# Kernel optimization log

Hardware: AMD Instinct MI355X
Metric: run time of the kernel (lower is better)

The kernel has to match this reference:

```python
import jax, jax.numpy as jnp
import numpy as np

B, T, C = 8, 1024, 768
H, D = 12, 64

def setup_inputs() -> dict:
    key = jax.random.key(0)
    ks = jax.random.split(key, 6)
    s = 0.02
    return {
        "x": jax.random.normal(ks[0], (B, T, C), dtype=jnp.float32),
        "Wq": jax.random.normal(ks[1], (H, C, D), dtype=jnp.float32) * s,
        "Wk": jax.random.normal(ks[2], (H, C, D), dtype=jnp.float32) * s,
        "Wv": jax.random.normal(ks[3], (H, C, D), dtype=jnp.float32) * s,
        "Wproj": jax.random.normal(ks[4], (C, C), dtype=jnp.float32) * s,
        "bproj": jnp.zeros((C,), dtype=jnp.float32),
    }

def reference(x, Wq, Wk, Wv, Wproj, bproj):
    # per-head projections, vectorized over heads: [B,H,T,D]
    q = jnp.einsum('btc,hcd->bhtd', x, Wq)
    k = jnp.einsum('btc,hcd->bhtd', x, Wk)
    v = jnp.einsum('btc,hcd->bhtd', x, Wv)
    scale = 1.0 / jnp.sqrt(jnp.asarray(q.shape[-1], q.dtype))
    scores = jnp.einsum('bhtd,bhsd->bhts', q, k) * scale  # [B,H,T,T]
    attn = jax.nn.softmax(scores, axis=-1)
    out = jnp.einsum('bhts,bhsd->bhtd', attn, v)          # [B,H,T,D]
    # concat heads along last dim -> [B,T,H*D]
    out = out.transpose(0, 2, 1, 3).reshape(x.shape[0], x.shape[1], -1)
    return out @ Wproj + bproj
```

## Files before the change

### kernel.cpp

```cpp
#include <hip/hip_runtime.h>
#include <hip/hip_bf16.h>

using u16 = unsigned short;

typedef __attribute__((ext_vector_type(8))) short bf16x8;
typedef __attribute__((ext_vector_type(4))) float f32x4;
typedef __attribute__((ext_vector_type(16))) float f32x16;

#define B_ 8
#define T_ 1024
#define C_ 768
#define H_ 12
#define D_ 64

typedef const void __attribute__((address_space(1))) gv_t;
typedef void __attribute__((address_space(3))) lv_t;

__device__ __forceinline__ void gload_lds16(const void* g, void* l) {
  __builtin_amdgcn_global_load_lds((gv_t*)g, (lv_t*)l, 16, 0, 0);
}

__device__ __forceinline__ u16 f2b(float f) {
  union { float f; unsigned u; } a; a.f = f;
  unsigned r = a.u + 0x7FFFu + ((a.u >> 16) & 1u);
  return (u16)(r >> 16);
}

__device__ __forceinline__ unsigned cvtpk_bf16(float lo, float hi) {
  unsigned r;
  asm("v_cvt_pk_bf16_f32 %0, %1, %2" : "=v"(r) : "v"(lo), "v"(hi));
  return r;
}
__device__ __forceinline__ void plane32_swap(unsigned &a, unsigned &b) {
  asm volatile("v_permlane32_swap_b32 %0, %1" : "+v"(a), "+v"(b));
}

__global__ __launch_bounds__(256) void prep_all(
    const float* __restrict__ x,
    const float* __restrict__ Wq, const float* __restrict__ Wk,
    const float* __restrict__ Wv, const float* __restrict__ Wp,
    u16* __restrict__ Xb, u16* __restrict__ Wqkvt, u16* __restrict__ Wpt)
{
  int bb = blockIdx.x;
  if (bb < 3072) {
    int i = (bb * 256 + threadIdx.x) * 8;
    float4 a = *(const float4*)(x + i);
    float4 b = *(const float4*)(x + i + 4);
    union { bf16x8 v; u16 s[8]; } o;
    o.s[0] = f2b(a.x); o.s[1] = f2b(a.y); o.s[2] = f2b(a.z); o.s[3] = f2b(a.w);
    o.s[4] = f2b(b.x); o.s[5] = f2b(b.y); o.s[6] = f2b(b.z); o.s[7] = f2b(b.w);
    *(bf16x8*)(Xb + i) = o.v;
  } else {
    int idx = (bb - 3072) * 256 + threadIdx.x;
    int p = idx / 589824;
    int r = idx - p * 589824;
    int n = r / 768, c = r - n * 768;
    if (p < 3) {
      const float* W = (p == 0) ? Wq : ((p == 1) ? Wk : Wv);
      int h = n >> 6, d = n & 63;
      Wqkvt[idx] = f2b(W[(size_t)h * (C_ * D_) + (size_t)c * D_ + d]);
    } else {
      Wpt[r] = f2b(Wp[(size_t)c * 768 + n]);
    }
  }
}

#define GEMM_MAINLOOP(APTR, BPTR, KDIM)                                          \
  for (int k0 = 0; k0 < (KDIM); k0 += 64) {                                      \
    _Pragma("unroll")                                                            \
    for (int q = 0; q < 4; ++q) {                                                \
      int db = q * 4096 + t * 16;                                                \
      int row = db >> 7;                                                         \
      int cb = (db ^ ((row & 7) << 4)) & 127;                                    \
      gload_lds16((const char*)(APTR) + ((size_t)(m0 + row) * (KDIM) + k0) * 2 + cb, \
                  (char*)As + db);                                               \
      gload_lds16((const char*)(BPTR) + ((size_t)(n0 + row) * (KDIM) + k0) * 2 + cb, \
                  (char*)Bs + db);                                               \
    }                                                                            \
    asm volatile("s_waitcnt vmcnt(0)" ::: "memory");                             \
    __syncthreads();                                                             \
    _Pragma("unroll")                                                            \
    for (int kq = 0; kq < 2; ++kq) {                                             \
      bf16x8 af[4], bfr[4];                                                      \
      _Pragma("unroll")                                                          \
      for (int i = 0; i < 4; ++i) {                                              \
        int ra = wr + i * 16 + lr;                                               \
        int Ua = ra * 128 + kq * 64 + hc;                                        \
        af[i] = *(const bf16x8*)((const char*)As + (Ua ^ ((ra & 7) << 4)));      \
        int rb = wc + i * 16 + lr;                                               \
        int Ub = rb * 128 + kq * 64 + hc;                                        \
        bfr[i] = *(const bf16x8*)((const char*)Bs + (Ub ^ ((rb & 7) << 4)));     \
      }                                                                          \
      _Pragma("unroll")                                                          \
      for (int i = 0; i < 4; ++i)                                                \
        _Pragma("unroll")                                                        \
        for (int j = 0; j < 4; ++j)                                              \
          acc[i][j] = __builtin_amdgcn_mfma_f32_16x16x32_bf16(af[i], bfr[j],     \
                                                              acc[i][j], 0, 0, 0); \
    }                                                                            \
    __syncthreads();                                                             \
  }

__global__ __launch_bounds__(256) void gemm_qkv(
    const u16* __restrict__ X, const u16* __restrict__ Wt,
    u16* __restrict__ Qw, u16* __restrict__ Kw, u16* __restrict__ Vt)
{
  __shared__ __align__(16) u16 As[128 * 64];
  __shared__ __align__(16) u16 Bs[128 * 64];
  const int t = threadIdx.x;
  const int l = t & 63, w = t >> 6;
  const int lr = l & 15;
  const int hc = (l >> 4) * 16;
  const int m0 = blockIdx.x * 128;
  const int n0 = blockIdx.y * 128;
  const int wr = (w >> 1) * 64, wc = (w & 1) * 64;

  f32x4 acc[4][4] = {};
  GEMM_MAINLOOP(X, Wt, 768)

  #pragma unroll
  for (int j = 0; j < 4; ++j) {
    int col_g = n0 + wc + j * 16 + lr;
    int p = (col_g >= 1536) ? 2 : ((col_g >= 768) ? 1 : 0);
    int rr = col_g - p * 768;
    int h = rr >> 6, d = rr & 63;
    #pragma unroll
    for (int i = 0; i < 4; ++i) {
      int rg0 = m0 + wr + i * 16 + ((l >> 4) << 2);
      int b = rg0 >> 10, tt = rg0 & 1023;
      if (p == 0) {
        size_t base = (((size_t)b * H_ + h) * T_ + tt) * D_ + d;
        #pragma unroll
        for (int r = 0; r < 4; ++r)
          Qw[base + (size_t)r * D_] = f2b(acc[i][j][r] * 0.18033688f);
      } else if (p == 1) {
        size_t base = (((size_t)b * H_ + h) * T_ + tt) * D_ + d;
        #pragma unroll
        for (int r = 0; r < 4; ++r) Kw[base + (size_t)r * D_] = f2b(acc[i][j][r]);
      } else {
        unsigned long long pk =
            (unsigned long long)f2b(acc[i][j][0]) |
            ((unsigned long long)f2b(acc[i][j][1]) << 16) |
            ((unsigned long long)f2b(acc[i][j][2]) << 32) |
            ((unsigned long long)f2b(acc[i][j][3]) << 48);
        *reinterpret_cast<unsigned long long*>(
            &Vt[(((size_t)b * H_ + h) * D_ + d) * T_ + tt]) = pk;
      }
    }
  }
}

__global__ __launch_bounds__(256) void gemm_proj(
    const u16* __restrict__ A, const u16* __restrict__ Wt,
    const float* __restrict__ bias, float* __restrict__ O)
{
  __shared__ __align__(16) u16 As[128 * 64];
  __shared__ __align__(16) u16 Bs[128 * 64];
  const int t = threadIdx.x;
  const int l = t & 63, w = t >> 6;
  const int lr = l & 15;
  const int hc = (l >> 4) * 16;
  const int m0 = blockIdx.x * 128;
  const int n0 = blockIdx.y * 128;
  const int wr = (w >> 1) * 64, wc = (w & 1) * 64;

  f32x4 acc[4][4] = {};
  GEMM_MAINLOOP(A, Wt, 768)

  #pragma unroll
  for (int j = 0; j < 4; ++j) {
    int col_g = n0 + wc + j * 16 + lr;
    float bb = bias[col_g];
    #pragma unroll
    for (int i = 0; i < 4; ++i) {
      int rg0 = m0 + wr + i * 16 + ((l >> 4) << 2);
      #pragma unroll
      for (int r = 0; r < 4; ++r)
        O[(size_t)(rg0 + r) * C_ + col_g] = acc[i][j][r] + bb;
    }
  }
}

__global__ __launch_bounds__(256) void attn_fwd(
    const u16* __restrict__ Qw, const u16* __restrict__ Kw,
    const u16* __restrict__ VT, u16* __restrict__ AO)
{
  __shared__ __align__(16) u16 Ks[2][64 * 64];
  __shared__ __align__(16) u16 Vs[2][64 * 64];
  const int t = threadIdx.x, w = t >> 6, l = t & 63;
  const int lq = l & 31, lh = l >> 5;

  const int bid = blockIdx.x;
  const int bh = (bid & 7) * 12 + ((bid >> 3) >> 3);
  const int qt = (bid >> 3) & 7;
  const int b = bh / H_, h = bh - b * H_;
  const u16* Qh = Qw + (size_t)bh * (T_ * D_);
  const char* Kp = (const char*)(Kw + (size_t)bh * (T_ * D_));
  const char* Vp = (const char*)(VT + (size_t)bh * (D_ * T_));
  const int q0w = qt * 128 + w * 32;
  const int qrow = q0w + lq;

  bf16x8 qf[4];
  #pragma unroll
  for (int ks = 0; ks < 4; ++ks)
    qf[ks] = *(const bf16x8*)(Qh + (size_t)qrow * D_ + lh * 8 + ks * 16);

  f32x16 oA = {}, oB = {};
  float mrun = -1e30f, lrun = 0.f;

  const int db0 = t * 16, db1 = 4096 + t * 16;
  const int row0 = db0 >> 7, row1 = db1 >> 7;
  const int cb0 = (db0 ^ ((row0 & 7) << 4)) & 127;
  const int cb1 = (db1 ^ ((row1 & 7) << 4)) & 127;

#define ISSUE_TILE(KT, BUF)                                                     \
  gload_lds16(Kp + (size_t)((KT) + row0) * 128 + cb0, (char*)Ks[BUF] + db0);    \
  gload_lds16(Kp + (size_t)((KT) + row1) * 128 + cb1, (char*)Ks[BUF] + db1);    \
  gload_lds16(Vp + (size_t)row0 * 2048 + (KT) * 2 + cb0, (char*)Vs[BUF] + db0); \
  gload_lds16(Vp + (size_t)row1 * 2048 + (KT) * 2 + cb1, (char*)Vs[BUF] + db1);

  ISSUE_TILE(0, 0)

  for (int kt_i = 0; kt_i < 16; ++kt_i) {
    const int cur = kt_i & 1;
    asm volatile("s_waitcnt vmcnt(0)" ::: "memory");
    __syncthreads();
    if (kt_i < 15) { ISSUE_TILE((kt_i + 1) * 64, cur ^ 1) }

    f32x16 sA = {}, sB = {};
    {
      bf16x8 ka[4];
      #pragma unroll
      for (int ks = 0; ks < 4; ++ks) {
        int row = lq;
        int U = row * 128 + ks * 32 + lh * 16;
        ka[ks] = *(const bf16x8*)((const char*)Ks[cur] + (U ^ ((row & 7) << 4)));
      }
      #pragma unroll
      for (int ks = 0; ks < 4; ++ks)
        sA = __builtin_amdgcn_mfma_f32_32x32x16_bf16(ka[ks], qf[ks], sA, 0, 0, 0);
      #pragma unroll
      for (int ks = 0; ks < 4; ++ks) {
        int row = lq + 32;
        int U = row * 128 + ks * 32 + lh * 16;
        ka[ks] = *(const bf16x8*)((const char*)Ks[cur] + (U ^ ((row & 7) << 4)));
      }
      #pragma unroll
      for (int ks = 0; ks < 4; ++ks)
        sB = __builtin_amdgcn_mfma_f32_32x32x16_bf16(ka[ks], qf[ks], sB, 0, 0, 0);
    }

    {
      float a16[16];
      #pragma unroll
      for (int r = 0; r < 16; ++r) a16[r] = fmaxf(sA[r], sB[r]);
      #pragma unroll
      for (int stp = 8; stp > 0; stp >>= 1)
        #pragma unroll
        for (int r = 0; r < stp; ++r) a16[r] = fmaxf(a16[r], a16[r + stp]);
      float mx = fmaxf(a16[0], __shfl_xor(a16[0], 32));
      if (!__all(mx <= mrun + 8.0f)) {
        float nm = fmaxf(mrun, mx);
        float alpha = exp2f(mrun - nm);
        mrun = nm;
        lrun *= alpha;
        #pragma unroll
        for (int r = 0; r < 16; ++r) { oA[r] *= alpha; oB[r] *= alpha; }
      }
      #pragma unroll
      for (int r = 0; r < 16; ++r) {
        sA[r] = exp2f(sA[r] - mrun);
        sB[r] = exp2f(sB[r] - mrun);
      }
      #pragma unroll
      for (int r = 0; r < 16; ++r) a16[r] = sA[r] + sB[r];
      #pragma unroll
      for (int stp = 8; stp > 0; stp >>= 1)
        #pragma unroll
        for (int r = 0; r < stp; ++r) a16[r] += a16[r + stp];
      lrun += a16[0] + __shfl_xor(a16[0], 32);
    }

    bf16x8 pb[4];
    #pragma unroll
    for (int ks = 0; ks < 4; ++ks) {
      f32x16& S = (ks < 2) ? sA : sB;
      const int g = (ks & 1) * 8;
      unsigned a0 = cvtpk_bf16(S[g + 0], S[g + 1]);
      unsigned a1 = cvtpk_bf16(S[g + 2], S[g + 3]);
      unsigned b0 = cvtpk_bf16(S[g + 4], S[g + 5]);
      unsigned b1 = cvtpk_bf16(S[g + 6], S[g + 7]);
      plane32_swap(a0, b0);
      plane32_swap(a1, b1);
      union { unsigned wd[4]; bf16x8 v; } u;
      u.wd[0] = a0; u.wd[1] = a1; u.wd[2] = b0; u.wd[3] = b1;
      pb[ks] = u.v;
    }

    {
      bf16x8 va[4];
      #pragma unroll
      for (int ks = 0; ks < 4; ++ks) {
        int row = lq;
        int U = row * 128 + ks * 32 + lh * 16;
        va[ks] = *(const bf16x8*)((const char*)Vs[cur] + (U ^ ((row & 7) << 4)));
      }
      #pragma unroll
      for (int ks = 0; ks < 4; ++ks)
        oA = __builtin_amdgcn_mfma_f32_32x32x16_bf16(va[ks], pb[ks], oA, 0, 0, 0);
      #pragma unroll
      for (int ks = 0; ks < 4; ++ks) {
        int row = lq + 32;
        int U = row * 128 + ks * 32 + lh * 16;
        va[ks] = *(const bf16x8*)((const char*)Vs[cur] + (U ^ ((row & 7) << 4)));
      }
      #pragma unroll
      for (int ks = 0; ks < 4; ++ks)
        oB = __builtin_amdgcn_mfma_f32_32x32x16_bf16(va[ks], pb[ks], oB, 0, 0, 0);
    }
  }
#undef ISSUE_TILE

  float inv = 1.0f / lrun;
  size_t base = ((size_t)b * T_ + qrow) * C_ + h * D_;
  #pragma unroll
  for (int dh = 0; dh < 2; ++dh) {
    const f32x16& OO = dh ? oB : oA;
    #pragma unroll
    for (int g = 0; g < 4; ++g) {
      int d0 = 8 * g + 4 * lh + 32 * dh;
      unsigned long long pk =
          (unsigned long long)f2b(OO[4 * g + 0] * inv) |
          ((unsigned long long)f2b(OO[4 * g + 1] * inv) << 16) |
          ((unsigned long long)f2b(OO[4 * g + 2] * inv) << 32) |
          ((unsigned long long)f2b(OO[4 * g + 3] * inv) << 48);
      *reinterpret_cast<unsigned long long*>(&AO[base + d0]) = pk;
    }
  }
}

extern "C" void kernel_launch(void* const* d_in, const int* in_sizes, int n_in,
                              void* d_out, int out_size, void* d_ws, size_t ws_size,
                              hipStream_t stream) {
  (void)in_sizes; (void)n_in; (void)out_size;
  const float* x     = (const float*)d_in[0];
  const float* Wq    = (const float*)d_in[1];
  const float* Wk    = (const float*)d_in[2];
  const float* Wv    = (const float*)d_in[3];
  const float* Wproj = (const float*)d_in[4];
  const float* bproj = (const float*)d_in[5];

  const size_t NEEDED = 55050240;
  if (ws_size < NEEDED) return;

  char* ws = (char*)d_ws;
  u16* Wpt   = (u16*)(ws);
  u16* Qw    = (u16*)(ws + 1179648);
  u16* Kw    = (u16*)(ws + 13762560);
  u16* Vt    = (u16*)(ws + 26345472);
  u16* Xb    = (u16*)(ws + 38928384);
  u16* AO    = (u16*)(ws + 38928384);
  u16* Wqkvt = (u16*)(ws + 51511296);

  prep_all<<<dim3(12288), dim3(256), 0, stream>>>(x, Wq, Wk, Wv, Wproj, Xb, Wqkvt, Wpt);
  gemm_qkv<<<dim3(64, 18), dim3(256), 0, stream>>>(Xb, Wqkvt, Qw, Kw, Vt);
  attn_fwd<<<dim3(768), dim3(256), 0, stream>>>(Qw, Kw, Vt, AO);
  gemm_proj<<<dim3(64, 6), dim3(256), 0, stream>>>(AO, Wpt, bproj, (float*)d_out);
}
```

Baseline: 151.1 us.

## Software-pipeline PV matmul one tile behind QK and compute row sums via MFMA

```diff
diff --git a/kernel.cpp b/kernel.cpp
--- a/kernel.cpp
+++ b/kernel.cpp
@@ -186,8 +186,8 @@
     const u16* __restrict__ VT, u16* __restrict__ AO)
 {
   __shared__ __align__(16) u16 Ks[2][64 * 64];
-  __shared__ __align__(16) u16 Vs[2][64 * 64];
-  const int t = threadIdx.x, w = t >> 6, l = t & 63;
+  __shared__ __align__(16) u16 Vs[3][64 * 64];
+  const int t = threadIdx.x, l = t & 63;
   const int lq = l & 31, lh = l >> 5;
 
   const int bid = blockIdx.x;
@@ -197,7 +197,7 @@
   const u16* Qh = Qw + (size_t)bh * (T_ * D_);
   const char* Kp = (const char*)(Kw + (size_t)bh * (T_ * D_));
   const char* Vp = (const char*)(VT + (size_t)bh * (D_ * T_));
-  const int q0w = qt * 128 + w * 32;
+  const int q0w = qt * 128 + (t >> 6) * 32;
   const int qrow = q0w + lq;
 
   bf16x8 qf[4];
@@ -205,27 +205,38 @@
   for (int ks = 0; ks < 4; ++ks)
     qf[ks] = *(const bf16x8*)(Qh + (size_t)qrow * D_ + lh * 8 + ks * 16);
 
-  f32x16 oA = {}, oB = {};
-  float mrun = -1e30f, lrun = 0.f;
+  bf16x8 ones;
+  {
+    union { u16 s[8]; bf16x8 v; } u;
+    #pragma unroll
+    for (int j = 0; j < 8; ++j) u.s[j] = 0x3F80;
+    ones = u.v;
+  }
+
+  f32x16 oA = {}, oB = {}, lacc = {};
+  float mrun = -1e30f;
+  bf16x8 pbP[4];
 
   const int db0 = t * 16, db1 = 4096 + t * 16;
   const int row0 = db0 >> 7, row1 = db1 >> 7;
   const int cb0 = (db0 ^ ((row0 & 7) << 4)) & 127;
   const int cb1 = (db1 ^ ((row1 & 7) << 4)) & 127;
 
-#define ISSUE_TILE(KT, BUF)                                                     \
-  gload_lds16(Kp + (size_t)((KT) + row0) * 128 + cb0, (char*)Ks[BUF] + db0);    \
-  gload_lds16(Kp + (size_t)((KT) + row1) * 128 + cb1, (char*)Ks[BUF] + db1);    \
-  gload_lds16(Vp + (size_t)row0 * 2048 + (KT) * 2 + cb0, (char*)Vs[BUF] + db0); \
-  gload_lds16(Vp + (size_t)row1 * 2048 + (KT) * 2 + cb1, (char*)Vs[BUF] + db1);
-
-  ISSUE_TILE(0, 0)
+#define ISSUE_TILE(KT, KB, VB)                                                   \
+  gload_lds16(Kp + (size_t)((KT) + row0) * 128 + cb0, (char*)Ks[KB] + db0);      \
+  gload_lds16(Kp + (size_t)((KT) + row1) * 128 + cb1, (char*)Ks[KB] + db1);      \
+  gload_lds16(Vp + (size_t)row0 * 2048 + (KT) * 2 + cb0, (char*)Vs[VB] + db0);   \
+  gload_lds16(Vp + (size_t)row1 * 2048 + (KT) * 2 + cb1, (char*)Vs[VB] + db1);
+
+  ISSUE_TILE(0, 0, 0)
+
+  int wv = 1, pv = 2;
 
   for (int kt_i = 0; kt_i < 16; ++kt_i) {
     const int cur = kt_i & 1;
     asm volatile("s_waitcnt vmcnt(0)" ::: "memory");
     __syncthreads();
-    if (kt_i < 15) { ISSUE_TILE((kt_i + 1) * 64, cur ^ 1) }
+    if (kt_i < 15) { ISSUE_TILE((kt_i + 1) * 64, cur ^ 1, wv) }
 
     f32x16 sA = {}, sB = {};
     {
@@ -248,6 +259,32 @@
       #pragma unroll
       for (int ks = 0; ks < 4; ++ks)
         sB = __builtin_amdgcn_mfma_f32_32x32x16_bf16(ka[ks], qf[ks], sB, 0, 0, 0);
+    }
+
+    if (kt_i > 0) {
+      const char* Vb = (const char*)Vs[pv];
+      bf16x8 va[4];
+      #pragma unroll
+      for (int ks = 0; ks < 4; ++ks) {
+        int row = lq;
+        int U = row * 128 + ks * 32 + lh * 16;
+        va[ks] = *(const bf16x8*)(Vb + (U ^ ((row & 7) << 4)));
+      }
+      #pragma unroll
+      for (int ks = 0; ks < 4; ++ks)
+        oA = __builtin_amdgcn_mfma_f32_32x32x16_bf16(va[ks], pbP[ks], oA, 0, 0, 0);
+      #pragma unroll
+      for (int ks = 0; ks < 4; ++ks) {
+        int row = lq + 32;
+        int U = row * 128 + ks * 32 + lh * 16;
+        va[ks] = *(const bf16x8*)(Vb + (U ^ ((row & 7) << 4)));
+      }
+      #pragma unroll
+      for (int ks = 0; ks < 4; ++ks)
+        oB = __builtin_amdgcn_mfma_f32_32x32x16_bf16(va[ks], pbP[ks], oB, 0, 0, 0);
+      #pragma unroll
+      for (int ks = 0; ks < 4; ++ks)
+        lacc = __builtin_amdgcn_mfma_f32_32x32x16_bf16(ones, pbP[ks], lacc, 0, 0, 0);
     }
 
     {
@@ -263,7 +300,7 @@
         float nm = fmaxf(mrun, mx);
         float alpha = exp2f(mrun - nm);
         mrun = nm;
-        lrun *= alpha;
+        lacc[0] *= alpha;
         #pragma unroll
         for (int r = 0; r < 16; ++r) { oA[r] *= alpha; oB[r] *= alpha; }
       }
@@ -272,16 +309,8 @@
         sA[r] = exp2f(sA[r] - mrun);
         sB[r] = exp2f(sB[r] - mrun);
       }
-      #pragma unroll
-      for (int r = 0; r < 16; ++r) a16[r] = sA[r] + sB[r];
-      #pragma unroll
-      for (int stp = 8; stp > 0; stp >>= 1)
-        #pragma unroll
-        for (int r = 0; r < stp; ++r) a16[r] += a16[r + stp];
-      lrun += a16[0] + __shfl_xor(a16[0], 32);
-    }
-
-    bf16x8 pb[4];
+    }
+
     #pragma unroll
     for (int ks = 0; ks < 4; ++ks) {
       f32x16& S = (ks < 2) ? sA : sB;
@@ -294,34 +323,41 @@
       plane32_swap(a1, b1);
       union { unsigned wd[4]; bf16x8 v; } u;
       u.wd[0] = a0; u.wd[1] = a1; u.wd[2] = b0; u.wd[3] = b1;
-      pb[ks] = u.v;
-    }
-
-    {
-      bf16x8 va[4];
-      #pragma unroll
-      for (int ks = 0; ks < 4; ++ks) {
-        int row = lq;
-        int U = row * 128 + ks * 32 + lh * 16;
-        va[ks] = *(const bf16x8*)((const char*)Vs[cur] + (U ^ ((row & 7) << 4)));
-      }
-      #pragma unroll
-      for (int ks = 0; ks < 4; ++ks)
-        oA = __builtin_amdgcn_mfma_f32_32x32x16_bf16(va[ks], pb[ks], oA, 0, 0, 0);
-      #pragma unroll
-      for (int ks = 0; ks < 4; ++ks) {
-        int row = lq + 32;
-        int U = row * 128 + ks * 32 + lh * 16;
-        va[ks] = *(const bf16x8*)((const char*)Vs[cur] + (U ^ ((row & 7) << 4)));
-      }
-      #pragma unroll
-      for (int ks = 0; ks < 4; ++ks)
-        oB = __builtin_amdgcn_mfma_f32_32x32x16_bf16(va[ks], pb[ks], oB, 0, 0, 0);
-    }
+      pbP[ks] = u.v;
+    }
+
+    wv = (wv == 2) ? 0 : wv + 1;
+    pv = (pv == 2) ? 0 : pv + 1;
   }
 #undef ISSUE_TILE
 
-  float inv = 1.0f / lrun;
+  {
+    const char* Vb = (const char*)Vs[pv];
+    bf16x8 va[4];
+    #pragma unroll
+    for (int ks = 0; ks < 4; ++ks) {
+      int row = lq;
+      int U = row * 128 + ks * 32 + lh * 16;
+      va[ks] = *(const bf16x8*)(Vb + (U ^ ((row & 7) << 4)));
+    }
+    #pragma unroll
+    for (int ks = 0; ks < 4; ++ks)
+      oA = __builtin_amdgcn_mfma_f32_32x32x16_bf16(va[ks], pbP[ks], oA, 0, 0, 0);
+    #pragma unroll
+    for (int ks = 0; ks < 4; ++ks) {
+      int row = lq + 32;
+      int U = row * 128 + ks * 32 + lh * 16;
+      va[ks] = *(const bf16x8*)(Vb + (U ^ ((row & 7) << 4)));
+    }
+    #pragma unroll
+    for (int ks = 0; ks < 4; ++ks)
+      oB = __builtin_amdgcn_mfma_f32_32x32x16_bf16(va[ks], pbP[ks], oB, 0, 0, 0);
+    #pragma unroll
+    for (int ks = 0; ks < 4; ++ks)
+      lacc = __builtin_amdgcn_mfma_f32_32x32x16_bf16(ones, pbP[ks], lacc, 0, 0, 0);
+  }
+
+  float inv = 1.0f / lacc[0];
   size_t base = ((size_t)b * T_ + qrow) * C_ + h * D_;
   #pragma unroll
   for (int dh = 0; dh < 2; ++dh) {
```

Result: no change. 150.1 us (-0.7%).
